# Performance work log

Hardware: AMD Instinct MI355X
Metric: run time of the kernel (lower is better)

Reference implementation:

```python
import jax, jax.numpy as jnp
import numpy as np

B, T, C = 2, 2048, 2048
N_HEAD, KV_HEADS = 16, 4
HEAD_DIM = C // N_HEAD  # 128
EPS = 1e-6


def setup_inputs() -> dict:
    key = jax.random.key(0)
    ks = jax.random.split(key, 3)
    x = jax.random.normal(ks[0], (B, T, C), dtype=jnp.float32)
    qkv_out = (N_HEAD + 2 * KV_HEADS) * HEAD_DIM  # 3072
    w_qkv = jax.random.normal(ks[1], (qkv_out, C), dtype=jnp.float32) * 0.02
    w_proj = jax.random.normal(ks[2], (C, C), dtype=jnp.float32) * 0.02
    q_norm_w = jnp.ones((HEAD_DIM,), dtype=jnp.float32)
    k_norm_w = jnp.ones((HEAD_DIM,), dtype=jnp.float32)
    # RoPE frequencies: theta = 10000^{-2i/d}, angles = pos * theta
    inv_freq = 1.0 / (10000.0 ** (np.arange(0, HEAD_DIM, 2, dtype=np.float32) / HEAD_DIM))
    angles = np.arange(T, dtype=np.float32)[:, None] * inv_freq[None, :]  # [T, 64]
    freqs_cos = jnp.asarray(np.cos(angles), dtype=jnp.float32)
    freqs_sin = jnp.asarray(np.sin(angles), dtype=jnp.float32)
    return {"x": x, "w_qkv": w_qkv, "w_proj": w_proj,
            "q_norm_w": q_norm_w, "k_norm_w": k_norm_w,
            "freqs_cos": freqs_cos, "freqs_sin": freqs_sin}


def _rope(t, cos, sin):
    # t: [B, H, T, D]; interpret last dim as D/2 complex pairs (a, b)
    a = t[..., 0::2]
    b = t[..., 1::2]
    oa = a * cos - b * sin
    ob = a * sin + b * cos
    return jnp.stack([oa, ob], axis=-1).reshape(t.shape)


def _rmsnorm(t, w, eps=EPS):
    rms = jnp.sqrt(jnp.mean(t * t, axis=-1, keepdims=True) + eps)
    return w * (t / rms)


def reference(x, w_qkv, w_proj, q_norm_w, k_norm_w, freqs_cos, freqs_sin):
    b, t, c = x.shape
    hd = HEAD_DIM
    qkv = x @ w_qkv.T  # [B, T, 3072]
    q_size = N_HEAD * hd
    kv_size = KV_HEADS * hd
    q = qkv[..., :q_size].reshape(b, t, N_HEAD, hd).transpose(0, 2, 1, 3)
    k = qkv[..., q_size:q_size + kv_size].reshape(b, t, KV_HEADS, hd).transpose(0, 2, 1, 3)
    v = qkv[..., q_size + kv_size:].reshape(b, t, KV_HEADS, hd).transpose(0, 2, 1, 3)
    # repeat_interleave KV heads to match query heads (GQA)
    rep = N_HEAD // KV_HEADS
    k = jnp.repeat(k, rep, axis=1)
    v = jnp.repeat(v, rep, axis=1)
    # RoPE (applied after repeat, matching the torch code order)
    cos = freqs_cos[:t][None, None, :, :]
    sin = freqs_sin[:t][None, None, :, :]
    q = _rope(q, cos, sin)
    k = _rope(k, cos, sin)
    # QK RMSNorm per head_dim
    q = _rmsnorm(q, q_norm_w)
    k = _rmsnorm(k, k_norm_w)
    # causal SDPA
    scores = jnp.einsum('bhqd,bhkd->bhqk', q, k) / jnp.sqrt(jnp.float32(hd))
    causal = jnp.tril(jnp.ones((t, t), dtype=bool))
    scores = jnp.where(causal[None, None], scores, jnp.finfo(scores.dtype).min)
    att = jax.nn.softmax(scores, axis=-1)
    y = jnp.einsum('bhqk,bhkd->bhqd', att, v)
    y = y.transpose(0, 2, 1, 3).reshape(b, t, c)
    return y @ w_proj.T
```

## Files before the change

### kernel.cpp

```cpp
#include <hip/hip_runtime.h>
#include <hip/hip_bf16.h>

#define B_    2
#define T_    2048
#define C_    2048
#define NH_   16
#define KVH_  4
#define HD_   128
#define QKV_  3072
#define M_    4096

typedef float  floatx4 __attribute__((ext_vector_type(4)));
typedef __bf16 bf16x8  __attribute__((ext_vector_type(8)));
typedef __bf16 bf16x4  __attribute__((ext_vector_type(4)));
typedef __bf16 bf16x2  __attribute__((ext_vector_type(2)));

typedef const __attribute__((address_space(1))) void* gas_t;
typedef __attribute__((address_space(3))) void*       las_t;
__device__ __forceinline__ void gl_lds16(const void* g, void* l) {
  __builtin_amdgcn_global_load_lds((gas_t)g, (las_t)l, 16, 0, 0);
}

__global__ __launch_bounds__(256) void cvt3(const float* __restrict__ s0, __bf16* __restrict__ d0, int n0,
                                            const float* __restrict__ s1, __bf16* __restrict__ d1, int n1,
                                            const float* __restrict__ s2, __bf16* __restrict__ d2, int n2) {
  int i = blockIdx.x * blockDim.x + threadIdx.x;
  const float* s; __bf16* d;
  if (i < n0) { s = s0; d = d0; }
  else {
    i -= n0;
    if (i < n1) { s = s1; d = d1; }
    else { i -= n1; if (i >= n2) return; s = s2; d = d2; }
  }
  float4 f = ((const float4*)s)[i];
  bf16x4 o = { (__bf16)f.x, (__bf16)f.y, (__bf16)f.z, (__bf16)f.w };
  ((bf16x4*)d)[i] = o;
}

template <typename OutT>
__global__ __launch_bounds__(256) void gemm_bt(const __bf16* __restrict__ A,
                                               const __bf16* __restrict__ Bm,
                                               OutT* __restrict__ Cc,
                                               int N, int K) {
  __shared__ __align__(16) __bf16 As[2][128 * 32];
  __shared__ __align__(16) __bf16 Bs[2][128 * 32];
  const int tid  = threadIdx.x;
  const int wid  = tid >> 6, lane = tid & 63, quad = lane >> 4, r16 = lane & 15;
  const int bm   = blockIdx.y * 128, bn = blockIdx.x * 128;
  const int wm   = (wid >> 1) * 64, wn = (wid & 1) * 64;
  const int srow = wid * 16 + (lane >> 2);
  const int scol = (lane & 3) * 8;
  const __bf16* aptr = A  + (size_t)(bm + srow) * K + scol;
  const __bf16* bptr = Bm + (size_t)(bn + srow) * K + scol;
  const size_t rowskip = (size_t)64 * K;

  floatx4 acc[4][4];
  #pragma unroll
  for (int i = 0; i < 4; i++)
    #pragma unroll
    for (int j = 0; j < 4; j++) acc[i][j] = (floatx4){0.f, 0.f, 0.f, 0.f};

  for (int k0 = 0; k0 < K; k0 += 64) {
    #pragma unroll
    for (int hf = 0; hf < 2; hf++) {
      gl_lds16(aptr + k0 + hf * 32,           &As[hf][wid * 512]);
      gl_lds16(aptr + rowskip + k0 + hf * 32, &As[hf][2048 + wid * 512]);
      gl_lds16(bptr + k0 + hf * 32,           &Bs[hf][wid * 512]);
      gl_lds16(bptr + rowskip + k0 + hf * 32, &Bs[hf][2048 + wid * 512]);
    }
    __syncthreads();

    #pragma unroll
    for (int hf = 0; hf < 2; hf++) {
      bf16x8 af[4], bfr[4];
      #pragma unroll
      for (int i = 0; i < 4; i++) af[i]  = *(const bf16x8*)&As[hf][(wm + i * 16 + r16) * 32 + quad * 8];
      #pragma unroll
      for (int j = 0; j < 4; j++) bfr[j] = *(const bf16x8*)&Bs[hf][(wn + j * 16 + r16) * 32 + quad * 8];
      #pragma unroll
      for (int i = 0; i < 4; i++)
        #pragma unroll
        for (int j = 0; j < 4; j++)
          acc[i][j] = __builtin_amdgcn_mfma_f32_16x16x32_bf16(af[i], bfr[j], acc[i][j], 0, 0, 0);
    }
    __syncthreads();
  }

  #pragma unroll
  for (int i = 0; i < 4; i++) {
    #pragma unroll
    for (int reg = 0; reg < 4; reg++) {
      int row = bm + wm + i * 16 + quad * 4 + reg;
      OutT* crow = Cc + (size_t)row * N + bn + wn;
      #pragma unroll
      for (int j = 0; j < 4; j++) crow[j * 16 + r16] = (OutT)acc[i][j][reg];
    }
  }
}

__global__ __launch_bounds__(256) void rope_norm(const __bf16* __restrict__ qkv,
                                                 const float* __restrict__ qw,
                                                 const float* __restrict__ kw,
                                                 const float* __restrict__ fc,
                                                 const float* __restrict__ fs,
                                                 __bf16* __restrict__ qn,
                                                 __bf16* __restrict__ kn) {
  const int tid  = threadIdx.x;
  const int wid  = tid >> 6, lane = tid & 63;
  const int row  = blockIdx.x * 4 + wid;
  const int b    = row >> 11, t = row & (T_ - 1);
  const float cs = fc[t * 64 + lane], sn = fs[t * 64 + lane];
  const __bf16* base = qkv + (size_t)row * QKV_;

  #pragma unroll 2
  for (int h = 0; h < NH_; h++) {
    bf16x2 ab = *(const bf16x2*)(base + h * HD_ + 2 * lane);
    float ax = (float)ab[0], ay = (float)ab[1];
    float oa = ax * cs - ay * sn;
    float ob = ax * sn + ay * cs;
    float ss = oa * oa + ob * ob;
    #pragma unroll
    for (int off = 32; off; off >>= 1) ss += __shfl_xor(ss, off);
    float rinv = rsqrtf(ss * (1.0f / HD_) + 1e-6f);
    bf16x2 o = { (__bf16)(oa * rinv * qw[2 * lane]), (__bf16)(ob * rinv * qw[2 * lane + 1]) };
    *(bf16x2*)&qn[(size_t)((b * NH_ + h) * T_ + t) * HD_ + 2 * lane] = o;
  }
  #pragma unroll 2
  for (int h = 0; h < KVH_; h++) {
    bf16x2 ab = *(const bf16x2*)(base + C_ + h * HD_ + 2 * lane);
    float ax = (float)ab[0], ay = (float)ab[1];
    float oa = ax * cs - ay * sn;
    float ob = ax * sn + ay * cs;
    float ss = oa * oa + ob * ob;
    #pragma unroll
    for (int off = 32; off; off >>= 1) ss += __shfl_xor(ss, off);
    float rinv = rsqrtf(ss * (1.0f / HD_) + 1e-6f);
    bf16x2 o = { (__bf16)(oa * rinv * kw[2 * lane]), (__bf16)(ob * rinv * kw[2 * lane + 1]) };
    *(bf16x2*)&kn[(size_t)((b * KVH_ + h) * T_ + t) * HD_ + 2 * lane] = o;
  }
}

__global__ __launch_bounds__(256) void vtrans(const __bf16* __restrict__ qkv,
                                              __bf16* __restrict__ vT) {
  __shared__ __bf16 L[64 * 68];
  const int tid = threadIdx.x;
  const int t0 = blockIdx.x * 64;
  const int d0 = blockIdx.y * 64;
  const int z  = blockIdx.z;
  const int b  = z >> 2, hk = z & 3;
  const int srcc = C_ + KVH_ * HD_ + hk * HD_ + d0;
  const int rr = tid >> 4, c4 = (tid & 15) * 4;
  #pragma unroll
  for (int i = 0; i < 4; i++) {
    int t = rr + i * 16;
    bf16x4 f = *(const bf16x4*)&qkv[(size_t)(b * T_ + t0 + t) * QKV_ + srcc + c4];
    *(bf16x4*)&L[t * 68 + c4] = f;
  }
  __syncthreads();
  const int dr = tid >> 3, tc8 = (tid & 7) * 8;
  #pragma unroll
  for (int i = 0; i < 2; i++) {
    int d = dr + i * 32;
    bf16x8 ov;
    #pragma unroll
    for (int j = 0; j < 8; j++) ov[j] = L[(tc8 + j) * 68 + d];
    *(bf16x8*)&vT[(size_t)(z * HD_ + d0 + d) * T_ + t0 + tc8] = ov;
  }
}

__device__ __forceinline__ void kv_prefetch8(const __bf16* kbase, const __bf16* vbase,
                                             int kt0, int wid, int lane,
                                             bf16x8 kreg[2], bf16x8 vreg[2]) {
  const int r4 = lane >> 2, c8 = (lane & 3) * 8;
  #pragma unroll
  for (int i = 0; i < 2; i++) {
    const int n = wid * 2 + i;
    kreg[i] = *(const bf16x8*)&kbase[(size_t)(kt0 + (n >> 2) * 16 + r4) * HD_ + (n & 3) * 32 + c8];
    vreg[i] = *(const bf16x8*)&vbase[(size_t)((n >> 1) * 16 + r4) * T_ + kt0 + (n & 1) * 32 + c8];
  }
}

__device__ __forceinline__ void kv_commit8(__bf16* Ks, __bf16* Vs, int wid, int lane,
                                           const bf16x8 kreg[2], const bf16x8 vreg[2]) {
  #pragma unroll
  for (int i = 0; i < 2; i++) {
    *(bf16x8*)(Ks + (wid * 2 + i) * 512 + lane * 8) = kreg[i];
    *(bf16x8*)(Vs + (wid * 2 + i) * 512 + lane * 8) = vreg[i];
  }
}

__global__ __launch_bounds__(512, 4) void flash(const __bf16* __restrict__ q,
                                                const __bf16* __restrict__ k,
                                                const __bf16* __restrict__ vT,
                                                __bf16* __restrict__ y) {
  __shared__ __align__(16) __bf16 Ks[64 * 128];
  __shared__ __align__(16) __bf16 Vs[128 * 64];
  __shared__ __align__(16) __bf16 Ps[8][16 * 72];
  const int tid = threadIdx.x;
  const int wid = tid >> 6, lane = tid & 63, quad = lane >> 4, r16 = lane & 15;
  const int x   = blockIdx.x;
  const int p   = (x >> 5) & 7, hl = x & 31;
  const int qt  = (x < 256) ? (15 - p) : p;
  const int b = hl >> 4, h = hl & 15, hk = h >> 2;

  const __bf16* kbase = k  + (size_t)(b * KVH_ + hk) * T_ * HD_;
  const __bf16* vbase = vT + (size_t)(b * KVH_ + hk) * HD_ * T_;
  __bf16* Pw = Ps[wid];
  const float sc = 0.08838834764831845f;
  const float NEG = -__builtin_inff();
  bf16x8 ones;
  #pragma unroll
  for (int i = 0; i < 8; i++) ones[i] = (__bf16)1.0f;

  const int nt = 2 * (qt + 1);
  const int r0 = qt * 128 + wid * 16;

  const __bf16* qrow = q + ((size_t)(b * NH_ + h) * T_ + r0 + r16) * HD_;
  bf16x8 qf[4];
  #pragma unroll
  for (int kb = 0; kb < 4; kb++) qf[kb] = *(const bf16x8*)&qrow[kb * 32 + quad * 8];

  floatx4 o[8], ol = (floatx4){0.f, 0.f, 0.f, 0.f};
  #pragma unroll
  for (int j = 0; j < 8; j++) o[j] = (floatx4){0.f, 0.f, 0.f, 0.f};
  float m_r[4] = {NEG, NEG, NEG, NEG};

  bf16x8 kreg[2], vreg[2];
  kv_prefetch8(kbase, vbase, 0, wid, lane, kreg, vreg);

  #pragma unroll 1
  for (int it = 0; it < nt; ++it) {
    __syncthreads();
    kv_commit8(Ks, Vs, wid, lane, kreg, vreg);
    __syncthreads();
    if (it + 1 < nt) kv_prefetch8(kbase, vbase, (it + 1) * 64, wid, lane, kreg, vreg);

    const int kt0 = it * 64;
    if (kt0 <= r0 + 15) {
      floatx4 s[4];
      #pragma unroll
      for (int cb = 0; cb < 4; cb++) s[cb] = (floatx4){0.f, 0.f, 0.f, 0.f};
      #pragma unroll
      for (int kb = 0; kb < 4; kb++)
        #pragma unroll
        for (int cb = 0; cb < 4; cb++) {
          bf16x8 kf = *(const bf16x8*)&Ks[(cb * 4 + kb) * 512 + r16 * 32 + quad * 8];
          s[cb] = __builtin_amdgcn_mfma_f32_16x16x32_bf16(qf[kb], kf, s[cb], 0, 0, 0);
        }

      const bool needmask = (kt0 + 63 > r0);
      float alpha[4];
      #pragma unroll
      for (int reg = 0; reg < 4; reg++) {
        const int rowq = r0 + quad * 4 + reg;
        float v0 = s[0][reg] * sc, v1 = s[1][reg] * sc;
        float v2 = s[2][reg] * sc, v3 = s[3][reg] * sc;
        if (needmask) {
          if (kt0 +      r16 > rowq) v0 = NEG;
          if (kt0 + 16 + r16 > rowq) v1 = NEG;
          if (kt0 + 32 + r16 > rowq) v2 = NEG;
          if (kt0 + 48 + r16 > rowq) v3 = NEG;
        }
        float mx = fmaxf(fmaxf(v0, v1), fmaxf(v2, v3));
        #pragma unroll
        for (int off = 8; off; off >>= 1) mx = fmaxf(mx, __shfl_xor(mx, off));
        float mnew = fmaxf(m_r[reg], mx);
        alpha[reg] = __expf(m_r[reg] - mnew);
        m_r[reg] = mnew;
        Pw[(quad * 4 + reg) * 72 +      r16] = (__bf16)__expf(v0 - mnew);
        Pw[(quad * 4 + reg) * 72 + 16 + r16] = (__bf16)__expf(v1 - mnew);
        Pw[(quad * 4 + reg) * 72 + 32 + r16] = (__bf16)__expf(v2 - mnew);
        Pw[(quad * 4 + reg) * 72 + 48 + r16] = (__bf16)__expf(v3 - mnew);
      }
      #pragma unroll
      for (int reg = 0; reg < 4; reg++) {
        ol[reg] *= alpha[reg];
        #pragma unroll
        for (int j = 0; j < 8; j++) o[j][reg] *= alpha[reg];
      }
      __asm__ volatile("" ::: "memory");
      bf16x8 pf0 = *(const bf16x8*)&Pw[r16 * 72 + quad * 8];
      bf16x8 pf1 = *(const bf16x8*)&Pw[r16 * 72 + 32 + quad * 8];
      ol = __builtin_amdgcn_mfma_f32_16x16x32_bf16(pf0, ones, ol, 0, 0, 0);
      ol = __builtin_amdgcn_mfma_f32_16x16x32_bf16(pf1, ones, ol, 0, 0, 0);
      #pragma unroll
      for (int j = 0; j < 8; j++) {
        bf16x8 vf0 = *(const bf16x8*)&Vs[(j * 2 + 0) * 512 + r16 * 32 + quad * 8];
        bf16x8 vf1 = *(const bf16x8*)&Vs[(j * 2 + 1) * 512 + r16 * 32 + quad * 8];
        o[j] = __builtin_amdgcn_mfma_f32_16x16x32_bf16(pf0, vf0, o[j], 0, 0, 0);
        o[j] = __builtin_amdgcn_mfma_f32_16x16x32_bf16(pf1, vf1, o[j], 0, 0, 0);
      }
    }
  }

  #pragma unroll
  for (int reg = 0; reg < 4; reg++) {
    int trow = r0 + quad * 4 + reg;
    float inv = 1.0f / ol[reg];
    __bf16* yr = y + ((size_t)(b * T_) + trow) * C_ + h * HD_;
    #pragma unroll
    for (int j = 0; j < 8; j++) yr[j * 16 + r16] = (__bf16)(o[j][reg] * inv);
  }
}

extern "C" void kernel_launch(void* const* d_in, const int* in_sizes, int n_in,
                              void* d_out, int out_size, void* d_ws, size_t ws_size,
                              hipStream_t stream) {
  const float* x     = (const float*)d_in[0];
  const float* wqkv  = (const float*)d_in[1];
  const float* wproj = (const float*)d_in[2];
  const float* qw    = (const float*)d_in[3];
  const float* kw    = (const float*)d_in[4];
  const float* fc    = (const float*)d_in[5];
  const float* fs    = (const float*)d_in[6];
  float* out = (float*)d_out;

  char* w = (char*)d_ws;
  __bf16* xb     = (__bf16*)w; w += (size_t)M_ * C_ * 2;
  __bf16* wqkvb  = (__bf16*)w; w += (size_t)QKV_ * C_ * 2;
  __bf16* wprojb = (__bf16*)w; w += (size_t)C_ * C_ * 2;
  __bf16* qkv    = (__bf16*)w; w += (size_t)M_ * QKV_ * 2;
  __bf16* qn     = (__bf16*)w; w += (size_t)B_ * NH_ * T_ * HD_ * 2;
  __bf16* kn     = (__bf16*)w; w += (size_t)B_ * KVH_ * T_ * HD_ * 2;
  __bf16* vT     = (__bf16*)w; w += (size_t)B_ * KVH_ * T_ * HD_ * 2;
  __bf16* ybf    = (__bf16*)w; w += (size_t)M_ * C_ * 2;

  const int n0 = M_ * C_ / 4, n1 = QKV_ * C_ / 4, n2 = C_ * C_ / 4;
  cvt3<<<(n0 + n1 + n2 + 255) / 256, 256, 0, stream>>>(x, xb, n0, wqkv, wqkvb, n1, wproj, wprojb, n2);

  gemm_bt<__bf16><<<dim3(QKV_ / 128, M_ / 128), 256, 0, stream>>>(xb, wqkvb, qkv, QKV_, C_);
  rope_norm<<<M_ / 4, 256, 0, stream>>>(qkv, qw, kw, fc, fs, qn, kn);
  vtrans<<<dim3(T_ / 64, HD_ / 64, B_ * KVH_), 256, 0, stream>>>(qkv, vT);
  flash<<<dim3(512), 512, 0, stream>>>(qn, kn, vT, ybf);
  gemm_bt<float><<<dim3(C_ / 128, M_ / 128), 256, 0, stream>>>(ybf, wprojb, out, C_, C_);
}
```

Baseline: 323.1 us.

## Give each flash wave 32 query rows and swizzle K/V shared-memory layout

The flash kernel now uses 4 waves of 256 threads, with each wave handling two 16-row query groups. Every K and V fragment read from shared memory now feeds two MFMAs, which halves LDS traffic per unit of compute. K/V staging uses an XOR swizzle on both write and read to cut bank conflicts. The cost is much higher register pressure from doubled accumulators and fewer waves per block, which may reduce occupancy and latency hiding.

Measured after the change: 353.6 us. 1.09x slower.

```diff
diff --git a/kernel.cpp b/kernel.cpp
--- a/kernel.cpp
+++ b/kernel.cpp
@@ -168,34 +168,42 @@
   }
 }
 
-__device__ __forceinline__ void kv_prefetch8(const __bf16* kbase, const __bf16* vbase,
-                                             int kt0, int wid, int lane,
-                                             bf16x8 kreg[2], bf16x8 vreg[2]) {
+__device__ __forceinline__ int swz_w(int lane) {
+  return ((lane & 3) << 4) | ((lane >> 2) ^ ((lane & 3) << 1));
+}
+__device__ __forceinline__ int swz_r(int quad, int r16) {
+  return (quad << 4) | (r16 ^ (quad << 1));
+}
+
+__device__ __forceinline__ void kv_prefetch16(const __bf16* kbase, const __bf16* vbase,
+                                              int kt0, int wid, int lane,
+                                              bf16x8 kreg[4], bf16x8 vreg[4]) {
   const int r4 = lane >> 2, c8 = (lane & 3) * 8;
   #pragma unroll
-  for (int i = 0; i < 2; i++) {
-    const int n = wid * 2 + i;
+  for (int i = 0; i < 4; i++) {
+    const int n = wid * 4 + i;
     kreg[i] = *(const bf16x8*)&kbase[(size_t)(kt0 + (n >> 2) * 16 + r4) * HD_ + (n & 3) * 32 + c8];
     vreg[i] = *(const bf16x8*)&vbase[(size_t)((n >> 1) * 16 + r4) * T_ + kt0 + (n & 1) * 32 + c8];
   }
 }
 
-__device__ __forceinline__ void kv_commit8(__bf16* Ks, __bf16* Vs, int wid, int lane,
-                                           const bf16x8 kreg[2], const bf16x8 vreg[2]) {
-  #pragma unroll
-  for (int i = 0; i < 2; i++) {
-    *(bf16x8*)(Ks + (wid * 2 + i) * 512 + lane * 8) = kreg[i];
-    *(bf16x8*)(Vs + (wid * 2 + i) * 512 + lane * 8) = vreg[i];
-  }
-}
-
-__global__ __launch_bounds__(512, 4) void flash(const __bf16* __restrict__ q,
+__device__ __forceinline__ void kv_commit16(__bf16* Ks, __bf16* Vs, int wid, int lane,
+                                            const bf16x8 kreg[4], const bf16x8 vreg[4]) {
+  const int slot = swz_w(lane);
+  #pragma unroll
+  for (int i = 0; i < 4; i++) {
+    *(bf16x8*)(Ks + (wid * 4 + i) * 512 + slot * 8) = kreg[i];
+    *(bf16x8*)(Vs + (wid * 4 + i) * 512 + slot * 8) = vreg[i];
+  }
+}
+
+__global__ __launch_bounds__(256, 2) void flash(const __bf16* __restrict__ q,
                                                 const __bf16* __restrict__ k,
                                                 const __bf16* __restrict__ vT,
                                                 __bf16* __restrict__ y) {
   __shared__ __align__(16) __bf16 Ks[64 * 128];
   __shared__ __align__(16) __bf16 Vs[128 * 64];
-  __shared__ __align__(16) __bf16 Ps[8][16 * 72];
+  __shared__ __align__(16) __bf16 Ps[4][32 * 72];
   const int tid = threadIdx.x;
   const int wid = tid >> 6, lane = tid & 63, quad = lane >> 4, r16 = lane & 15;
   const int x   = blockIdx.x;
@@ -213,94 +221,120 @@
   for (int i = 0; i < 8; i++) ones[i] = (__bf16)1.0f;
 
   const int nt = 2 * (qt + 1);
-  const int r0 = qt * 128 + wid * 16;
-
-  const __bf16* qrow = q + ((size_t)(b * NH_ + h) * T_ + r0 + r16) * HD_;
-  bf16x8 qf[4];
-  #pragma unroll
-  for (int kb = 0; kb < 4; kb++) qf[kb] = *(const bf16x8*)&qrow[kb * 32 + quad * 8];
-
-  floatx4 o[8], ol = (floatx4){0.f, 0.f, 0.f, 0.f};
-  #pragma unroll
-  for (int j = 0; j < 8; j++) o[j] = (floatx4){0.f, 0.f, 0.f, 0.f};
-  float m_r[4] = {NEG, NEG, NEG, NEG};
-
-  bf16x8 kreg[2], vreg[2];
-  kv_prefetch8(kbase, vbase, 0, wid, lane, kreg, vreg);
+  const int r0 = qt * 128 + wid * 32;
+
+  bf16x8 qf[2][4];
+  #pragma unroll
+  for (int rg = 0; rg < 2; rg++) {
+    const __bf16* qrow = q + ((size_t)(b * NH_ + h) * T_ + r0 + rg * 16 + r16) * HD_;
+    #pragma unroll
+    for (int kb = 0; kb < 4; kb++) qf[rg][kb] = *(const bf16x8*)&qrow[kb * 32 + quad * 8];
+  }
+
+  floatx4 o[2][8], ol[2];
+  float m_r[2][4];
+  #pragma unroll
+  for (int rg = 0; rg < 2; rg++) {
+    ol[rg] = (floatx4){0.f, 0.f, 0.f, 0.f};
+    #pragma unroll
+    for (int j = 0; j < 8; j++) o[rg][j] = (floatx4){0.f, 0.f, 0.f, 0.f};
+    #pragma unroll
+    for (int reg = 0; reg < 4; reg++) m_r[rg][reg] = NEG;
+  }
+
+  bf16x8 kreg[4], vreg[4];
+  kv_prefetch16(kbase, vbase, 0, wid, lane, kreg, vreg);
 
   #pragma unroll 1
   for (int it = 0; it < nt; ++it) {
     __syncthreads();
-    kv_commit8(Ks, Vs, wid, lane, kreg, vreg);
+    kv_commit16(Ks, Vs, wid, lane, kreg, vreg);
     __syncthreads();
-    if (it + 1 < nt) kv_prefetch8(kbase, vbase, (it + 1) * 64, wid, lane, kreg, vreg);
+    if (it + 1 < nt) kv_prefetch16(kbase, vbase, (it + 1) * 64, wid, lane, kreg, vreg);
 
     const int kt0 = it * 64;
-    if (kt0 <= r0 + 15) {
-      floatx4 s[4];
-      #pragma unroll
-      for (int cb = 0; cb < 4; cb++) s[cb] = (floatx4){0.f, 0.f, 0.f, 0.f};
+    if (kt0 <= r0 + 31) {
+      floatx4 s[2][4];
+      #pragma unroll
+      for (int rg = 0; rg < 2; rg++)
+        #pragma unroll
+        for (int cb = 0; cb < 4; cb++) s[rg][cb] = (floatx4){0.f, 0.f, 0.f, 0.f};
       #pragma unroll
       for (int kb = 0; kb < 4; kb++)
         #pragma unroll
         for (int cb = 0; cb < 4; cb++) {
-          bf16x8 kf = *(const bf16x8*)&Ks[(cb * 4 + kb) * 512 + r16 * 32 + quad * 8];
-          s[cb] = __builtin_amdgcn_mfma_f32_16x16x32_bf16(qf[kb], kf, s[cb], 0, 0, 0);
+          bf16x8 kf = *(const bf16x8*)&Ks[(cb * 4 + kb) * 512 + swz_r(quad, r16) * 8];
+          #pragma unroll
+          for (int rg = 0; rg < 2; rg++)
+            s[rg][cb] = __builtin_amdgcn_mfma_f32_16x16x32_bf16(qf[rg][kb], kf, s[rg][cb], 0, 0, 0);
         }
 
-      const bool needmask = (kt0 + 63 > r0);
-      float alpha[4];
-      #pragma unroll
-      for (int reg = 0; reg < 4; reg++) {
-        const int rowq = r0 + quad * 4 + reg;
-        float v0 = s[0][reg] * sc, v1 = s[1][reg] * sc;
-        float v2 = s[2][reg] * sc, v3 = s[3][reg] * sc;
-        if (needmask) {
-          if (kt0 +      r16 > rowq) v0 = NEG;
-          if (kt0 + 16 + r16 > rowq) v1 = NEG;
-          if (kt0 + 32 + r16 > rowq) v2 = NEG;
-          if (kt0 + 48 + r16 > rowq) v3 = NEG;
+      float alpha[2][4];
+      #pragma unroll
+      for (int rg = 0; rg < 2; rg++) {
+        const bool needmask = (kt0 + 63 > r0 + rg * 16);
+        #pragma unroll
+        for (int reg = 0; reg < 4; reg++) {
+          const int rowq = r0 + rg * 16 + quad * 4 + reg;
+          float v0 = s[rg][0][reg] * sc, v1 = s[rg][1][reg] * sc;
+          float v2 = s[rg][2][reg] * sc, v3 = s[rg][3][reg] * sc;
+          if (needmask) {
+            if (kt0 +      r16 > rowq) v0 = NEG;
+            if (kt0 + 16 + r16 > rowq) v1 = NEG;
+            if (kt0 + 32 + r16 > rowq) v2 = NEG;
+            if (kt0 + 48 + r16 > rowq) v3 = NEG;
+          }
+          float mx = fmaxf(fmaxf(v0, v1), fmaxf(v2, v3));
+          #pragma unroll
+          for (int off = 8; off; off >>= 1) mx = fmaxf(mx, __shfl_xor(mx, off));
+          float mnew = fmaxf(m_r[rg][reg], mx);
+          alpha[rg][reg] = __expf(m_r[rg][reg] - mnew);
+          m_r[rg][reg] = mnew;
+          const int prow = rg * 16 + quad * 4 + reg;
+          Pw[prow * 72 +      r16] = (__bf16)__expf(v0 - mnew);
+          Pw[prow * 72 + 16 + r16] = (__bf16)__expf(v1 - mnew);
+          Pw[prow * 72 + 32 + r16] = (__bf16)__expf(v2 - mnew);
+          Pw[prow * 72 + 48 + r16] = (__bf16)__expf(v3 - mnew);
         }
-        float mx = fmaxf(fmaxf(v0, v1), fmaxf(v2, v3));
-        #pragma unroll
-        for (int off = 8; off; off >>= 1) mx = fmaxf(mx, __shfl_xor(mx, off));
-        float mnew = fmaxf(m_r[reg], mx);
-        alpha[reg] = __expf(m_r[reg] - mnew);
-        m_r[reg] = mnew;
-        Pw[(quad * 4 + reg) * 72 +      r16] = (__bf16)__expf(v0 - mnew);
-        Pw[(quad * 4 + reg) * 72 + 16 + r16] = (__bf16)__expf(v1 - mnew);
-        Pw[(quad * 4 + reg) * 72 + 32 + r16] = (__bf16)__expf(v2 - mnew);
-        Pw[(quad * 4 + reg) * 72 + 48 + r16] = (__bf16)__expf(v3 - mnew);
-      }
-      #pragma unroll
-      for (int reg = 0; reg < 4; reg++) {
-        ol[reg] *= alpha[reg];
-        #pragma unroll
-        for (int j = 0; j < 8; j++) o[j][reg] *= alpha[reg];
+        #pragma unroll
+        for (int reg = 0; reg < 4; reg++) {
+          ol[rg][reg] *= alpha[rg][reg];
+          #pragma unroll
+          for (int j = 0; j < 8; j++) o[rg][j][reg] *= alpha[rg][reg];
+        }
       }
       __asm__ volatile("" ::: "memory");
-      bf16x8 pf0 = *(const bf16x8*)&Pw[r16 * 72 + quad * 8];
-      bf16x8 pf1 = *(const bf16x8*)&Pw[r16 * 72 + 32 + quad * 8];
-      ol = __builtin_amdgcn_mfma_f32_16x16x32_bf16(pf0, ones, ol, 0, 0, 0);
-      ol = __builtin_amdgcn_mfma_f32_16x16x32_bf16(pf1, ones, ol, 0, 0, 0);
+      bf16x8 pf0[2], pf1[2];
+      #pragma unroll
+      for (int rg = 0; rg < 2; rg++) {
+        pf0[rg] = *(const bf16x8*)&Pw[(rg * 16 + r16) * 72 + quad * 8];
+        pf1[rg] = *(const bf16x8*)&Pw[(rg * 16 + r16) * 72 + 32 + quad * 8];
+        ol[rg] = __builtin_amdgcn_mfma_f32_16x16x32_bf16(pf0[rg], ones, ol[rg], 0, 0, 0);
+        ol[rg] = __builtin_amdgcn_mfma_f32_16x16x32_bf16(pf1[rg], ones, ol[rg], 0, 0, 0);
+      }
       #pragma unroll
       for (int j = 0; j < 8; j++) {
-        bf16x8 vf0 = *(const bf16x8*)&Vs[(j * 2 + 0) * 512 + r16 * 32 + quad * 8];
-        bf16x8 vf1 = *(const bf16x8*)&Vs[(j * 2 + 1) * 512 + r16 * 32 + quad * 8];
-        o[j] = __builtin_amdgcn_mfma_f32_16x16x32_bf16(pf0, vf0, o[j], 0, 0, 0);
-        o[j] = __builtin_amdgcn_mfma_f32_16x16x32_bf16(pf1, vf1, o[j], 0, 0, 0);
+        bf16x8 vf0 = *(const bf16x8*)&Vs[(j * 2 + 0) * 512 + swz_r(quad, r16) * 8];
+        bf16x8 vf1 = *(const bf16x8*)&Vs[(j * 2 + 1) * 512 + swz_r(quad, r16) * 8];
+        #pragma unroll
+        for (int rg = 0; rg < 2; rg++) {
+          o[rg][j] = __builtin_amdgcn_mfma_f32_16x16x32_bf16(pf0[rg], vf0, o[rg][j], 0, 0, 0);
+          o[rg][j] = __builtin_amdgcn_mfma_f32_16x16x32_bf16(pf1[rg], vf1, o[rg][j], 0, 0, 0);
+        }
       }
     }
   }
 
   #pragma unroll
-  for (int reg = 0; reg < 4; reg++) {
-    int trow = r0 + quad * 4 + reg;
-    float inv = 1.0f / ol[reg];
-    __bf16* yr = y + ((size_t)(b * T_) + trow) * C_ + h * HD_;
-    #pragma unroll
-    for (int j = 0; j < 8; j++) yr[j * 16 + r16] = (__bf16)(o[j][reg] * inv);
-  }
+  for (int rg = 0; rg < 2; rg++)
+    #pragma unroll
+    for (int reg = 0; reg < 4; reg++) {
+      int trow = r0 + rg * 16 + quad * 4 + reg;
+      float inv = 1.0f / ol[rg][reg];
+      __bf16* yr = y + ((size_t)(b * T_) + trow) * C_ + h * HD_;
+      #pragma unroll
+      for (int j = 0; j < 8; j++) yr[j * 16 + r16] = (__bf16)(o[rg][j][reg] * inv);
+    }
 }
 
 extern "C" void kernel_launch(void* const* d_in, const int* in_sizes, int n_in,
@@ -331,6 +365,6 @@
   gemm_bt<__bf16><<<dim3(QKV_ / 128, M_ / 128), 256, 0, stream>>>(xb, wqkvb, qkv, QKV_, C_);
   rope_norm<<<M_ / 4, 256, 0, stream>>>(qkv, qw, kw, fc, fs, qn, kn);
   vtrans<<<dim3(T_ / 64, HD_ / 64, B_ * KVH_), 256, 0, stream>>>(qkv, vT);
-  flash<<<dim3(512), 512, 0, stream>>>(qn, kn, vT, ybf);
+  flash<<<dim3(512), 256, 0, stream>>>(qn, kn, vT, ybf);
   gemm_bt<float><<<dim3(C_ / 128, M_ / 128), 256, 0, stream>>>(ybf, wprojb, out, C_, C_);
 }
```
